# Kernel tuning notes

Hardware: AMD Instinct MI355X
Metric: run time of the kernel (lower is better)

Reference implementation:

```python
import jax, jax.numpy as jnp
import numpy as np


def setup_inputs() -> dict:
    key = jax.random.key(0)
    k1, k2, k3, k4 = jax.random.split(key, 4)
    N, E, C_in, C_out = 50000, 625000, 256, 128
    x = jax.random.normal(k1, (N, C_in), dtype=jnp.float32)
    W = jax.random.normal(k2, (C_out, C_in), dtype=jnp.float32) * (1.0 / np.sqrt(C_in))
    b = jax.random.normal(k3, (C_out,), dtype=jnp.float32) * 0.01
    edge_index = jax.random.randint(k4, (2, E), 0, N, dtype=jnp.int64)
    return {"x": x, "W": W, "b": b, "edge_index": edge_index}


def reference(x, W, b, edge_index):
    # x: [N, C_in], W: [C_out, C_in], b: [C_out], edge_index: [2, E]
    N = x.shape[0]
    h = jnp.dot(x, W.T) + b  # [N, C_out] (nn.Linear)
    r, c = edge_index[0], edge_index[1]
    # node degree via scatter_add of ones over destination index r
    deg = jax.ops.segment_sum(jnp.ones(r.shape[0], dtype=h.dtype), r, num_segments=N)
    # rsqrt with inf (deg==0) replaced by 0
    nd_rsqrt = jnp.where(deg > 0, jax.lax.rsqrt(jnp.maximum(deg, 1.0)), jnp.zeros_like(deg))
    # gather messages from source nodes c, normalize by source rsqrt-degree
    message_norm = h[c] * nd_rsqrt[c][:, None]  # [E, C_out]
    # scatter-add to destination nodes r
    out = jax.ops.segment_sum(message_norm, r, num_segments=N)  # [N, C_out]
    # final destination-side normalization
    return out * nd_rsqrt[:, None]
```

## Files before the change

kernel.cpp:

```cpp
#include <hip/hip_runtime.h>

#define C_IN 256
#define C_OUT 128
#define ELL_PAD 64
#define FILL_EPT 8

typedef __attribute__((ext_vector_type(8))) short bf16x8;
typedef __attribute__((ext_vector_type(4))) short short4v;
typedef __attribute__((ext_vector_type(4))) float f32x4;

__device__ inline unsigned short f2bf(float f) {
    unsigned u = __builtin_bit_cast(unsigned, f);
    unsigned r = (u + 0x7FFFu + ((u >> 16) & 1u)) >> 16;
    return (unsigned short)r;
}
__device__ inline float bflo(unsigned u) { return __builtin_bit_cast(float, u << 16); }
__device__ inline float bfhi(unsigned u) { return __builtin_bit_cast(float, u & 0xFFFF0000u); }

__global__ __launch_bounds__(256) void wconv_zero_kernel(const float* __restrict__ W,
                                                         unsigned short* __restrict__ WB,
                                                         int* __restrict__ cursor, int N) {
    int ci = blockIdx.x * 256 + threadIdx.x;
    int q = ci & 3, cl = (ci >> 2) & 15, ctt = ci >> 6;
    int colw = (ctt & 7) * 16 + cl;
    int k0 = (ctt >> 3) * 32 + q * 8;
    const float* src = W + colw * C_IN + k0;
    bf16x8 o;
    #pragma unroll
    for (int j = 0; j < 8; ++j) o[j] = (short)f2bf(src[j]);
    *(bf16x8*)(WB + (size_t)ci * 8) = o;
    for (int k = ci; k < N; k += 4096) cursor[k] = 0;
}

__global__ __launch_bounds__(256) void fused_fill_gemm(const float* __restrict__ x,
                                                       const unsigned short* __restrict__ WB,
                                                       const float* __restrict__ b,
                                                       const int* __restrict__ ridx,
                                                       const int* __restrict__ cidx,
                                                       int* __restrict__ cursor,
                                                       unsigned short* __restrict__ col_ell,
                                                       unsigned short* __restrict__ h,
                                                       int N, int E, int G_fill) {
    __shared__ char xs[64 * 512];
    int tid = threadIdx.x;

    int T = gridDim.x;
    long long i = blockIdx.x;
    int f_i  = (int)((i * (long long)G_fill) / T);
    int f_i1 = (int)(((i + 1) * (long long)G_fill) / T);

    if (f_i1 > f_i) {
        int base = f_i * (256 * FILL_EPT) + tid;
        #pragma unroll
        for (int k = 0; k < FILL_EPT; ++k) {
            int e = base + k * 256;
            if (e < E) {
                int r = ridx[e];
                int c = cidx[e];
                int pos = atomicAdd(&cursor[r], 1);
                if (pos < ELL_PAD)
                    col_ell[(size_t)r * ELL_PAD + pos] = (unsigned short)c;
            }
        }
        return;
    }

    int gemmId = (int)i - f_i;
    int w = tid >> 6, l = tid & 63;
    int row0 = gemmId * 64;

    #pragma unroll
    for (int it = 0; it < 16; ++it) {
        int row = it * 4 + w;
        int grow = row0 + row;
        float4 v = make_float4(0.f, 0.f, 0.f, 0.f);
        if (grow < N) v = *(const float4*)(x + (size_t)grow * C_IN + l * 4);
        short4v sv;
        sv.x = (short)f2bf(v.x); sv.y = (short)f2bf(v.y);
        sv.z = (short)f2bf(v.z); sv.w = (short)f2bf(v.w);
        int inrow = (l * 8) ^ ((row & 7) << 4);
        *(short4v*)(xs + row * 512 + inrow) = sv;
    }
    __syncthreads();

    int lq = l >> 4, lr = l & 15;
    int arow = w * 16 + lr;
    int aswz = (arow & 7) << 4;
    const char* xrow = xs + arow * 512;
    const char* wb = (const char*)WB;
    int boff = lr * 64 + lq * 16;

    f32x4 acc[8];
    #pragma unroll
    for (int ct = 0; ct < 8; ++ct) acc[ct] = (f32x4){0.f, 0.f, 0.f, 0.f};

    #pragma unroll
    for (int t = 0; t < 8; ++t) {
        int inrow = (t * 64 + lq * 16) ^ aswz;
        bf16x8 af = *(const bf16x8*)(xrow + inrow);
        #pragma unroll
        for (int ct = 0; ct < 8; ++ct) {
            bf16x8 bfv = *(const bf16x8*)(wb + (t * 8 + ct) * 1024 + boff);
            acc[ct] = __builtin_amdgcn_mfma_f32_16x16x32_bf16(af, bfv, acc[ct], 0, 0, 0);
        }
    }

    #pragma unroll
    for (int ct = 0; ct < 8; ++ct) {
        int colc = ct * 16 + lr;
        float bv = b[colc];
        #pragma unroll
        for (int r = 0; r < 4; ++r) {
            int grow = row0 + w * 16 + lq * 4 + r;
            if (grow < N)
                h[(size_t)grow * C_OUT + colc] = f2bf(acc[ct][r] + bv);
        }
    }
}

__global__ __launch_bounds__(256) void gather_kernel(const int* __restrict__ cursor,
                                                     const unsigned short* __restrict__ col_ell,
                                                     const unsigned short* __restrict__ h,
                                                     float* __restrict__ out, int N) {
    int gid = blockIdx.x * 256 + threadIdx.x;
    int node = gid >> 4;
    if (node >= N) return;
    int lane = gid & 15;

    int degN = cursor[node];
    float sv = (degN > 0) ? rsqrtf((float)degN) : 0.0f;
    int deg = (degN > ELL_PAD) ? ELL_PAD : degN;
    const unsigned short* cl = col_ell + (size_t)node * ELL_PAD;
    const char* hb = (const char*)h;

    float acc[8] = {0.f, 0.f, 0.f, 0.f, 0.f, 0.f, 0.f, 0.f};
    int i = 0;
    for (; i + 2 <= deg; i += 2) {
        int c0 = cl[i], c1 = cl[i + 1];
        uint4 v0 = *(const uint4*)(hb + (size_t)c0 * (C_OUT * 2) + lane * 16);
        uint4 v1 = *(const uint4*)(hb + (size_t)c1 * (C_OUT * 2) + lane * 16);
        int d0 = cursor[c0], d1 = cursor[c1];
        float s0 = (d0 > 0) ? rsqrtf((float)d0) : 0.0f;
        float s1 = (d1 > 0) ? rsqrtf((float)d1) : 0.0f;
        acc[0] += s0 * bflo(v0.x); acc[1] += s0 * bfhi(v0.x);
        acc[2] += s0 * bflo(v0.y); acc[3] += s0 * bfhi(v0.y);
        acc[4] += s0 * bflo(v0.z); acc[5] += s0 * bfhi(v0.z);
        acc[6] += s0 * bflo(v0.w); acc[7] += s0 * bfhi(v0.w);
        acc[0] += s1 * bflo(v1.x); acc[1] += s1 * bfhi(v1.x);
        acc[2] += s1 * bflo(v1.y); acc[3] += s1 * bfhi(v1.y);
        acc[4] += s1 * bflo(v1.z); acc[5] += s1 * bfhi(v1.z);
        acc[6] += s1 * bflo(v1.w); acc[7] += s1 * bfhi(v1.w);
    }
    if (i < deg) {
        int c0 = cl[i];
        uint4 v0 = *(const uint4*)(hb + (size_t)c0 * (C_OUT * 2) + lane * 16);
        int d0 = cursor[c0];
        float s0 = (d0 > 0) ? rsqrtf((float)d0) : 0.0f;
        acc[0] += s0 * bflo(v0.x); acc[1] += s0 * bfhi(v0.x);
        acc[2] += s0 * bflo(v0.y); acc[3] += s0 * bfhi(v0.y);
        acc[4] += s0 * bflo(v0.z); acc[5] += s0 * bfhi(v0.z);
        acc[6] += s0 * bflo(v0.w); acc[7] += s0 * bfhi(v0.w);
    }
    float4 o0 = make_float4(acc[0] * sv, acc[1] * sv, acc[2] * sv, acc[3] * sv);
    float4 o1 = make_float4(acc[4] * sv, acc[5] * sv, acc[6] * sv, acc[7] * sv);
    float* op = out + (size_t)node * C_OUT + lane * 8;
    *(float4*)(op)     = o0;
    *(float4*)(op + 4) = o1;
}

extern "C" void kernel_launch(void* const* d_in, const int* in_sizes, int n_in,
                              void* d_out, int out_size, void* d_ws, size_t ws_size,
                              hipStream_t stream) {
    const float* x = (const float*)d_in[0];
    const float* W = (const float*)d_in[1];
    const float* b = (const float*)d_in[2];
    const int*   ei = (const int*)d_in[3];
    float* out = (float*)d_out;

    int N = in_sizes[0] / C_IN;
    int E = in_sizes[3] / 2;
    const int* ridx = ei;
    const int* cidx = ei + E;

    char* wsc = (char*)d_ws;
    unsigned short* h  = (unsigned short*)wsc;       wsc += (size_t)N * C_OUT * sizeof(unsigned short);
    unsigned short* WB = (unsigned short*)wsc;       wsc += (size_t)C_OUT * C_IN * sizeof(unsigned short);
    int*   cursor   = (int*)wsc;                     wsc += (size_t)N * sizeof(int);
    unsigned short* col_ell = (unsigned short*)wsc;

    wconv_zero_kernel<<<16, 256, 0, stream>>>(W, WB, cursor, N);

    int G_fill = (E + 256 * FILL_EPT - 1) / (256 * FILL_EPT);
    int G_gemm = (N + 63) / 64;
    fused_fill_gemm<<<G_fill + G_gemm, 256, 0, stream>>>(x, WB, b, ridx, cidx,
                                                         cursor, col_ell, h, N, E, G_fill);

    long long gth = (long long)N * 16;
    gather_kernel<<<(int)((gth + 255) / 256), 256, 0, stream>>>(cursor, col_ell, h, out, N);
}
```

Baseline: 84.11 us.

## Load GEMM A-fragments directly from global memory and halve fill edges per thread

The GEMM blocks no longer stage x through shared memory with a barrier. Each lane now loads its own 8 floats per k-step straight from global memory, converts them to bf16 in registers and feeds the MFMA. This removes the LDS round trip and __syncthreads, and freeing the 32 KB of LDS may let more blocks fit per CU. Separately, FILL_EPT drops from 8 to 4, which doubles the number of fill blocks and spreads the atomic ELL fill more finely. The cost is less coalesced global reads for x, since each lane fetches 32-byte chunks from rows spaced 1 KB apart.

Result: slower. 91.16 us (+8.4%).

```diff
diff --git a/kernel.cpp b/kernel.cpp
--- a/kernel.cpp
+++ b/kernel.cpp
@@ -3,10 +3,9 @@
 #define C_IN 256
 #define C_OUT 128
 #define ELL_PAD 64
-#define FILL_EPT 8
+#define FILL_EPT 4
 
 typedef __attribute__((ext_vector_type(8))) short bf16x8;
-typedef __attribute__((ext_vector_type(4))) short short4v;
 typedef __attribute__((ext_vector_type(4))) float f32x4;
 
 __device__ inline unsigned short f2bf(float f) {
@@ -41,7 +40,6 @@
                                                        unsigned short* __restrict__ col_ell,
                                                        unsigned short* __restrict__ h,
                                                        int N, int E, int G_fill) {
-    __shared__ char xs[64 * 512];
     int tid = threadIdx.x;
 
     int T = gridDim.x;
@@ -68,25 +66,11 @@
     int gemmId = (int)i - f_i;
     int w = tid >> 6, l = tid & 63;
     int row0 = gemmId * 64;
+    int lq = l >> 4, lr = l & 15;
 
-    #pragma unroll
-    for (int it = 0; it < 16; ++it) {
-        int row = it * 4 + w;
-        int grow = row0 + row;
-        float4 v = make_float4(0.f, 0.f, 0.f, 0.f);
-        if (grow < N) v = *(const float4*)(x + (size_t)grow * C_IN + l * 4);
-        short4v sv;
-        sv.x = (short)f2bf(v.x); sv.y = (short)f2bf(v.y);
-        sv.z = (short)f2bf(v.z); sv.w = (short)f2bf(v.w);
-        int inrow = (l * 8) ^ ((row & 7) << 4);
-        *(short4v*)(xs + row * 512 + inrow) = sv;
-    }
-    __syncthreads();
-
-    int lq = l >> 4, lr = l & 15;
-    int arow = w * 16 + lr;
-    int aswz = (arow & 7) << 4;
-    const char* xrow = xs + arow * 512;
+    int arow = row0 + w * 16 + lr;
+    bool rowok = (arow < N);
+    const float* xr = x + (size_t)(rowok ? arow : 0) * C_IN + lq * 8;
     const char* wb = (const char*)WB;
     int boff = lr * 64 + lq * 16;
 
@@ -96,8 +80,17 @@
 
     #pragma unroll
     for (int t = 0; t < 8; ++t) {
-        int inrow = (t * 64 + lq * 16) ^ aswz;
-        bf16x8 af = *(const bf16x8*)(xrow + inrow);
+        float4 v0 = make_float4(0.f, 0.f, 0.f, 0.f);
+        float4 v1 = make_float4(0.f, 0.f, 0.f, 0.f);
+        if (rowok) {
+            v0 = *(const float4*)(xr + t * 32);
+            v1 = *(const float4*)(xr + t * 32 + 4);
+        }
+        bf16x8 af;
+        af[0] = (short)f2bf(v0.x); af[1] = (short)f2bf(v0.y);
+        af[2] = (short)f2bf(v0.z); af[3] = (short)f2bf(v0.w);
+        af[4] = (short)f2bf(v1.x); af[5] = (short)f2bf(v1.y);
+        af[6] = (short)f2bf(v1.z); af[7] = (short)f2bf(v1.w);
         #pragma unroll
         for (int ct = 0; ct < 8; ++ct) {
             bf16x8 bfv = *(const bf16x8*)(wb + (t * 8 + ct) * 1024 + boff);
```
